# Kernel optimization log

Hardware: AMD Instinct MI355X
Metric: run time of the kernel (lower is better)

Reference implementation:

```python
import jax, jax.numpy as jnp
import numpy as np

D = 1024
M = 32768
B = 4096
TEMP = 1.0
LN_EPS = 1e-5


def setup_inputs() -> dict:
    key = jax.random.key(0)
    ks = jax.random.split(key, 8)
    s = 1.0 / np.sqrt(D)
    return {
        "query": jax.random.normal(ks[0], (B, D), dtype=jnp.float32),
        "mem": jax.random.normal(ks[1], (M, D), dtype=jnp.float32),
        "Wq": jax.random.normal(ks[2], (D, D), dtype=jnp.float32) * s,
        "bq": jax.random.normal(ks[3], (D,), dtype=jnp.float32) * 0.01,
        "Wk": jax.random.normal(ks[4], (D, D), dtype=jnp.float32) * s,
        "bk": jax.random.normal(ks[5], (D,), dtype=jnp.float32) * 0.01,
        "Wv": jax.random.normal(ks[6], (D, D), dtype=jnp.float32) * s,
        "bv": jax.random.normal(ks[7], (D,), dtype=jnp.float32) * 0.01,
        "gamma": jnp.ones((D,), dtype=jnp.float32),
        "beta": jnp.zeros((D,), dtype=jnp.float32),
        "k": 8,
    }


def reference(query, mem, Wq, bq, Wk, bk, Wv, bv, gamma, beta, k):
    d = query.shape[-1]
    # Linear projections (torch Linear: x @ W.T + b)
    q = query @ Wq.T + bq            # [B, d]
    K = mem @ Wk.T + bk              # [M, d]
    V = mem @ Wv.T + bv              # [M, d]
    # Scaled similarity matrix
    sims = (q @ K.T) / (jnp.sqrt(jnp.asarray(d, q.dtype)) * TEMP)  # [B, M]
    # Top-k selection, then irregular gather of V rows
    _, topi = jax.lax.top_k(sims, k)  # [B, k]
    ret = V[topi]                     # [B, k, d]
    # LayerNorm over last dim (elementwise affine, eps=1e-5, biased var)
    mu = jnp.mean(ret, axis=-1, keepdims=True)
    var = jnp.var(ret, axis=-1, keepdims=True)
    return (ret - mu) * jax.lax.rsqrt(var + LN_EPS) * gamma + beta
```

## Files before the change

kernel.cpp:

```cpp
#include <hip/hip_runtime.h>
#include <hip/hip_bf16.h>
#include <math.h>

#define D_DIM 1024
#define B_ROWS 4096
#define M_ROWS 32768
#define TOPK 8
#define TOPC 16
#define TOPB 8
#define NCB (M_ROWS / 128)

#define BM 128
#define BN 64
#define BK 32

typedef __attribute__((ext_vector_type(8))) short bf16x8;
typedef __attribute__((ext_vector_type(4))) float f32x4;

__device__ __forceinline__ unsigned short f32_to_bf16(float f) {
  unsigned int u = __float_as_uint(f);
  unsigned int r = (u + 0x7FFFu + ((u >> 16) & 1u)) >> 16;
  return (unsigned short)r;
}
__device__ __forceinline__ float bf16_to_f32(unsigned short h) {
  return __uint_as_float(((unsigned int)h) << 16);
}
__device__ __forceinline__ void async_copy16(void* lds, const void* g) {
  __builtin_amdgcn_global_load_lds(
      (const __attribute__((address_space(1))) unsigned int*)g,
      (__attribute__((address_space(3))) unsigned int*)lds, 16, 0, 0);
}

template <int N>
__device__ __forceinline__ void insN(float v, int idx,
                                     float* __restrict__ tv,
                                     int* __restrict__ ti) {
  if (v < tv[N - 1]) return;
  if (v == tv[N - 1] && idx > ti[N - 1]) return;
  float cv = v;
  int ci = idx;
#pragma unroll
  for (int p = 0; p < N; ++p) {
    if (cv > tv[p] || (cv == tv[p] && ci < ti[p])) {
      const float t0 = tv[p]; tv[p] = cv; cv = t0;
      const int t1 = ti[p]; ti[p] = ci; ci = t1;
    }
  }
}

__global__ __launch_bounds__(256) void gram_f64(
    const float* __restrict__ Wq, const float* __restrict__ Wk,
    double* __restrict__ G)
{
  __shared__ float sA[32][68];
  __shared__ float sB[32][68];
  const int tid = threadIdx.x;
  const int tx = tid & 15, ty = tid >> 4;
  const int f0 = blockIdx.x * 64;
  const int e0 = blockIdx.y * 64;

  double acc[4][4];
#pragma unroll
  for (int i = 0; i < 4; ++i)
#pragma unroll
    for (int j = 0; j < 4; ++j) acc[i][j] = 0.0;

  for (int k0 = 0; k0 < D_DIM; k0 += 32) {
#pragma unroll
    for (int it = 0; it < 2; ++it) {
      const int L = it * 256 + tid;
      const int kk = L >> 4, c4 = (L & 15) * 4;
      *(float4*)&sA[kk][c4] = *(const float4*)(Wq + (size_t)(k0 + kk) * D_DIM + f0 + c4);
      *(float4*)&sB[kk][c4] = *(const float4*)(Wk + (size_t)(k0 + kk) * D_DIM + e0 + c4);
    }
    __syncthreads();
#pragma unroll
    for (int kk = 0; kk < 32; ++kk) {
      const double a[4] = {sA[kk][ty * 4 + 0], sA[kk][ty * 4 + 1],
                           sA[kk][ty * 4 + 2], sA[kk][ty * 4 + 3]};
      const double b[4] = {sB[kk][tx * 4 + 0], sB[kk][tx * 4 + 1],
                           sB[kk][tx * 4 + 2], sB[kk][tx * 4 + 3]};
#pragma unroll
      for (int i = 0; i < 4; ++i)
#pragma unroll
        for (int j = 0; j < 4; ++j)
          acc[i][j] = fma(a[i], b[j], acc[i][j]);
    }
    __syncthreads();
  }
#pragma unroll
  for (int i = 0; i < 4; ++i)
#pragma unroll
    for (int j = 0; j < 4; ++j)
      G[(size_t)(f0 + ty * 4 + i) * D_DIM + e0 + tx * 4 + j] = acc[i][j];
}

__global__ __launch_bounds__(256) void colred_f64(
    const float* __restrict__ W, const float* __restrict__ v,
    double* __restrict__ outv)
{
  const int c = blockIdx.x * 256 + threadIdx.x;
  double acc = 0.0;
  for (int n = 0; n < D_DIM; ++n)
    acc = fma((double)W[(size_t)n * D_DIM + c], (double)v[n], acc);
  outv[c] = acc;
}

__global__ __launch_bounds__(256) void dot1024_f64(
    const float* __restrict__ a, const float* __restrict__ b,
    double* __restrict__ out)
{
  const int tid = threadIdx.x;
  double acc = 0.0;
#pragma unroll
  for (int i = 0; i < 4; ++i) {
    const int idx = tid * 4 + i;
    acc = fma((double)a[idx], (double)b[idx], acc);
  }
#pragma unroll
  for (int off = 32; off > 0; off >>= 1) acc += __shfl_down(acc, off);
  __shared__ double red[4];
  if ((tid & 63) == 0) red[tid >> 6] = acc;
  __syncthreads();
  if (tid == 0) out[0] = red[0] + red[1] + red[2] + red[3];
}

__global__ __launch_bounds__(256) void qbk_w(
    const float* __restrict__ query, const double* __restrict__ w,
    const double* __restrict__ s0, double* __restrict__ qbk)
{
  const int b = blockIdx.x * 4 + (threadIdx.x >> 6);
  const int lane = threadIdx.x & 63;
  const float* qrow = query + (size_t)b * D_DIM + lane * 16;
  const double* wrow = w + lane * 16;
  double acc = 0.0;
#pragma unroll
  for (int i = 0; i < 16; ++i)
    acc = fma((double)qrow[i], wrow[i], acc);
#pragma unroll
  for (int off = 32; off > 0; off >>= 1) acc += __shfl_down(acc, off);
  if (lane == 0) qbk[b] = acc + s0[0];
}

__global__ __launch_bounds__(256) void uproj_G(
    const float* __restrict__ query, const double* __restrict__ G,
    const double* __restrict__ ubias, double* __restrict__ U)
{
  __shared__ double sAdT[32][130];
  __shared__ double sBd[32][68];
  const int tid = threadIdx.x;
  const int tx = tid & 15, ty = tid >> 4;
  const int row0 = blockIdx.x * 128;
  const int col0 = blockIdx.y * 64;

  double acc[2][4][4];
#pragma unroll
  for (int g = 0; g < 2; ++g)
#pragma unroll
    for (int i = 0; i < 4; ++i)
#pragma unroll
      for (int j = 0; j < 4; ++j) acc[g][i][j] = 0.0;

  for (int k0 = 0; k0 < D_DIM; k0 += 32) {
#pragma unroll
    for (int it = 0; it < 4; ++it) {
      const int L = it * 256 + tid;
      const int rowa = L >> 3, c4 = (L & 7) * 4;
      const float4 v =
          *(const float4*)(query + (size_t)(row0 + rowa) * D_DIM + k0 + c4);
      sAdT[c4 + 0][rowa] = (double)v.x;
      sAdT[c4 + 1][rowa] = (double)v.y;
      sAdT[c4 + 2][rowa] = (double)v.z;
      sAdT[c4 + 3][rowa] = (double)v.w;
    }
#pragma unroll
    for (int it = 0; it < 4; ++it) {
      const int L = it * 256 + tid;
      const int kk = L >> 5, c2 = (L & 31) * 2;
      *(double2*)&sBd[kk][c2] =
          *(const double2*)(G + (size_t)(k0 + kk) * D_DIM + col0 + c2);
    }
    __syncthreads();
#pragma unroll
    for (int kk = 0; kk < 32; ++kk) {
      const double2 p0 = *(const double2*)&sAdT[kk][ty * 4];
      const double2 p1 = *(const double2*)&sAdT[kk][ty * 4 + 2];
      const double2 p2 = *(const double2*)&sAdT[kk][64 + ty * 4];
      const double2 p3 = *(const double2*)&sAdT[kk][64 + ty * 4 + 2];
      const double a0[4] = {p0.x, p0.y, p1.x, p1.y};
      const double a1[4] = {p2.x, p2.y, p3.x, p3.y};
      const double bb[4] = {sBd[kk][tx * 4 + 0], sBd[kk][tx * 4 + 1],
                            sBd[kk][tx * 4 + 2], sBd[kk][tx * 4 + 3]};
#pragma unroll
      for (int i = 0; i < 4; ++i)
#pragma unroll
        for (int j = 0; j < 4; ++j) {
          acc[0][i][j] = fma(a0[i], bb[j], acc[0][i][j]);
          acc[1][i][j] = fma(a1[i], bb[j], acc[1][i][j]);
        }
    }
    __syncthreads();
  }
  const double ub[4] = {ubias[col0 + tx * 4 + 0], ubias[col0 + tx * 4 + 1],
                        ubias[col0 + tx * 4 + 2], ubias[col0 + tx * 4 + 3]};
#pragma unroll
  for (int g = 0; g < 2; ++g)
#pragma unroll
    for (int i = 0; i < 4; ++i) {
      const size_t base = (size_t)(row0 + g * 64 + ty * 4 + i) * D_DIM + col0 + tx * 4;
      *(double2*)(U + base)     = (double2){acc[g][i][0] + ub[0], acc[g][i][1] + ub[1]};
      *(double2*)(U + base + 2) = (double2){acc[g][i][2] + ub[2], acc[g][i][3] + ub[3]};
    }
}

#define SBUF3 12288
__global__ __launch_bounds__(512, 4) void sims_topc_gemm(
    const unsigned short* __restrict__ A, const unsigned short* __restrict__ B,
    float* __restrict__ part_v, int* __restrict__ part_i)
{
  __shared__ unsigned short smem[3 * SBUF3];

  const int tid = threadIdx.x;
  const int lane = tid & 63;
  const int wave = tid >> 6;
  const int wr = wave >> 1;
  const int wc = wave & 1;

  const int bid = blockIdx.x;
  const int x = bid & 7;
  const int t9 = bid >> 3;
  const int cbg = t9 >> 7;
  const int r = (t9 >> 3) & 15;
  const int cbl = t9 & 7;
  const int cb = (x * 4 + cbg) * 8 + cbl;
  const int row0 = r * 256;
  const int col0 = cb * 128;

  const int st_r = lane >> 2;
  const int st_swz = ((lane & 3) ^ ((st_r >> 1) & 3)) * 16;

  auto STAGE = [&](int d, int k0) {
    unsigned short* buf = smem + d * SBUF3;
#pragma unroll
    for (int i = 0; i < 3; ++i) {
      const int seg = wave * 3 + i;
      if (seg < 16) {
        const int grow = row0 + seg * 16 + st_r;
        async_copy16((char*)(buf + seg * 512),
                     (const char*)(A + (size_t)grow * D_DIM + k0) + st_swz);
      } else {
        const int s2 = seg - 16;
        const int grow = col0 + s2 * 16 + st_r;
        async_copy16((char*)(buf + 8192 + s2 * 512),
                     (const char*)(B + (size_t)grow * D_DIM + k0) + st_swz);
      }
    }
  };

  f32x4 acc[4][4];
#pragma unroll
  for (int m = 0; m < 4; ++m)
#pragma unroll
    for (int n = 0; n < 4; ++n) acc[m][n] = (f32x4){0.f, 0.f, 0.f, 0.f};

  auto COMPUTE = [&](int d) {
    const unsigned short* sA = smem + d * SBUF3;
    const unsigned short* sB = sA + 8192;
    bf16x8 af[4], bfr[4];
    const int ch = lane >> 4;
#pragma unroll
    for (int m = 0; m < 4; ++m) {
      const int Ra = wr * 64 + m * 16 + (lane & 15);
      af[m] = *(const bf16x8*)((const char*)sA + Ra * 64 + ((ch ^ ((Ra >> 1) & 3)) * 16));
    }
#pragma unroll
    for (int n = 0; n < 4; ++n) {
      const int Rb = wc * 64 + n * 16 + (lane & 15);
      bfr[n] = *(const bf16x8*)((const char*)sB + Rb * 64 + ((ch ^ ((Rb >> 1) & 3)) * 16));
    }
    __builtin_amdgcn_s_setprio(1);
#pragma unroll
    for (int m = 0; m < 4; ++m)
#pragma unroll
      for (int n = 0; n < 4; ++n)
        acc[m][n] = __builtin_amdgcn_mfma_f32_16x16x32_bf16(af[m], bfr[n], acc[m][n], 0, 0, 0);
    __builtin_amdgcn_s_setprio(0);
  };

  STAGE(0, 0);
  STAGE(1, 32);
  asm volatile("s_waitcnt vmcnt(3)" ::: "memory");
  __builtin_amdgcn_sched_barrier(0);
  __builtin_amdgcn_s_barrier();

  for (int tt = 0; tt < 30; tt += 3) {
    STAGE(2, (tt + 2) * 32);
    COMPUTE(0);
    asm volatile("s_waitcnt vmcnt(3)" ::: "memory");
    __builtin_amdgcn_sched_barrier(0);
    __builtin_amdgcn_s_barrier();

    STAGE(0, (tt + 3) * 32);
    COMPUTE(1);
    asm volatile("s_waitcnt vmcnt(3)" ::: "memory");
    __builtin_amdgcn_sched_barrier(0);
    __builtin_amdgcn_s_barrier();

    STAGE(1, (tt + 4) * 32);
    COMPUTE(2);
    asm volatile("s_waitcnt vmcnt(3)" ::: "memory");
    __builtin_amdgcn_sched_barrier(0);
    __builtin_amdgcn_s_barrier();
  }
  COMPUTE(0);
  asm volatile("s_waitcnt vmcnt(0)" ::: "memory");
  __builtin_amdgcn_sched_barrier(0);
  __builtin_amdgcn_s_barrier();
  COMPUTE(1);
  __builtin_amdgcn_sched_barrier(0);
  __builtin_amdgcn_s_barrier();

#pragma unroll
  for (int m = 0; m < 4; ++m)
#pragma unroll
    for (int n = 0; n < 4; ++n)
#pragma unroll
      for (int rg = 0; rg < 4; ++rg) {
        const int row = wr * 64 + m * 16 + (lane >> 4) * 4 + rg;
        const int colL = wc * 64 + n * 16 + (lane & 15);
        smem[row * 132 + colL] = f32_to_bf16(acc[m][n][rg]);
      }
  __syncthreads();

  {
    const int row = tid & 255;
    const int h = tid >> 8;
    float tv[4];
    int ti_[4];
#pragma unroll
    for (int p = 0; p < 4; ++p) { tv[p] = -INFINITY; ti_[p] = 0; }
    const unsigned short* crow = smem + row * 132 + h * 64;
    const int gcol = col0 + h * 64;
    for (int j = 0; j < 64; j += 4) {
      const ushort4 c4 = *(const ushort4*)(crow + j);
      insN<4>(bf16_to_f32(c4.x), gcol + j + 0, tv, ti_);
      insN<4>(bf16_to_f32(c4.y), gcol + j + 1, tv, ti_);
      insN<4>(bf16_to_f32(c4.z), gcol + j + 2, tv, ti_);
      insN<4>(bf16_to_f32(c4.w), gcol + j + 3, tv, ti_);
    }
    const size_t base = ((size_t)(row0 + row) * NCB + cb) * TOPB + h * 4;
    *(float4*)(part_v + base) = (float4){tv[0], tv[1], tv[2], tv[3]};
    *(int4*)(part_i + base)   = (int4){ti_[0], ti_[1], ti_[2], ti_[3]};
  }
}

__global__ __launch_bounds__(256) void merge_cand256(
    const float* __restrict__ part_v, const int* __restrict__ part_i,
    int* __restrict__ cand)
{
  const int r = blockIdx.x;
  const int tid = threadIdx.x;
  const int lane = tid & 63;
  const int wave = tid >> 6;

  float tv[8];
  int ti[8];
  {
    const size_t base = ((size_t)r * NCB + tid) * TOPB;
    const float4 a0 = *(const float4*)(part_v + base);
    const float4 a1 = *(const float4*)(part_v + base + 4);
    const int4 b0 = *(const int4*)(part_i + base);
    const int4 b1 = *(const int4*)(part_i + base + 4);
    tv[0] = a0.x; tv[1] = a0.y; tv[2] = a0.z; tv[3] = a0.w;
    tv[4] = a1.x; tv[5] = a1.y; tv[6] = a1.z; tv[7] = a1.w;
    ti[0] = b0.x; ti[1] = b0.y; ti[2] = b0.z; ti[3] = b0.w;
    ti[4] = b1.x; ti[5] = b1.y; ti[6] = b1.z; ti[7] = b1.w;
  }
  unsigned rem = 0xFFu;

  __shared__ float wv4[4];
  __shared__ int wi4[4];
  __shared__ int winner;

  for (int p = 0; p < TOPC; ++p) {
    float bv = -INFINITY;
    int bi = 0x7FFFFFFF;
#pragma unroll
    for (int e = 0; e < 8; ++e) {
      const bool alive = (rem >> e) & 1u;
      const float v = tv[e];
      const int ix = ti[e];
      if (alive && (v > bv || (v == bv && ix < bi))) { bv = v; bi = ix; }
    }
#pragma unroll
    for (int off = 32; off > 0; off >>= 1) {
      const float ov = __shfl_down(bv, off);
      const int oi = __shfl_down(bi, off);
      if (ov > bv || (ov == bv && oi < bi)) { bv = ov; bi = oi; }
    }
    if (lane == 0) { wv4[wave] = bv; wi4[wave] = bi; }
    __syncthreads();
    if (tid == 0) {
      float gv = wv4[0];
      int gi = wi4[0];
#pragma unroll
      for (int w = 1; w < 4; ++w)
        if (wv4[w] > gv || (wv4[w] == gv && wi4[w] < gi)) { gv = wv4[w]; gi = wi4[w]; }
      winner = gi;
      cand[(size_t)r * TOPC + p] = gi;
    }
    __syncthreads();
    const int wgi = winner;
#pragma unroll
    for (int e = 0; e < 8; ++e)
      if (ti[e] == wgi) rem &= ~(1u << e);
  }
}

__global__ __launch_bounds__(256) void rescore_topk_u(
    const double* __restrict__ U, const double* __restrict__ qbk,
    const float* __restrict__ mem, const int* __restrict__ cand,
    int* __restrict__ topi)
{
  const int b = blockIdx.x;
  const int tid = threadIdx.x;
  const int wave = tid >> 6;
  const int lane = tid & 63;

  __shared__ double sval[TOPC];
  __shared__ int sidx[TOPC];

  const double* urow = U + (size_t)b * D_DIM + lane * 16;
  double uv[16];
#pragma unroll
  for (int i = 0; i < 8; ++i) {
    const double2 d2 = *(const double2*)(urow + i * 2);
    uv[i * 2] = d2.x;
    uv[i * 2 + 1] = d2.y;
  }
  const double qb = qbk[b];

  for (int c = wave; c < TOPC; c += 4) {
    const int ci = cand[(size_t)b * TOPC + c];
    const float* mrow = mem + (size_t)ci * D_DIM + lane * 16;
    double acc = 0.0;
#pragma unroll
    for (int i = 0; i < 4; ++i) {
      const float4 mv = *(const float4*)(mrow + i * 4);
      acc = fma(uv[i * 4 + 0], (double)mv.x, acc);
      acc = fma(uv[i * 4 + 1], (double)mv.y, acc);
      acc = fma(uv[i * 4 + 2], (double)mv.z, acc);
      acc = fma(uv[i * 4 + 3], (double)mv.w, acc);
    }
#pragma unroll
    for (int off = 32; off > 0; off >>= 1) acc += __shfl_down(acc, off);
    if (lane == 0) { sval[c] = acc + qb; sidx[c] = ci; }
  }
  __syncthreads();

  if (tid == 0) {
    bool used[TOPC];
#pragma unroll
    for (int p = 0; p < TOPC; ++p) used[p] = false;
#pragma unroll
    for (int p = 0; p < TOPK; ++p) {
      int best = -1;
      double bv = 0.0;
      int bi = 0;
      for (int c = 0; c < TOPC; ++c) {
        if (used[c]) continue;
        const double v = sval[c];
        const int ix = sidx[c];
        if (best < 0 || v > bv || (v == bv && ix < bi)) { best = c; bv = v; bi = ix; }
      }
      used[best] = true;
      topi[(size_t)b * TOPK + p] = bi;
    }
  }
}

#define N4_MEM   (M_ROWS * D_DIM / 4)
#define N4_QUERY (B_ROWS * D_DIM / 4)
#define N4_W     (D_DIM * D_DIM / 4)
#define N4_TOTAL (N4_MEM + N4_QUERY + 3 * N4_W)

__global__ __launch_bounds__(256) void cast_all_bf16(
    const float* __restrict__ mem, const float* __restrict__ query,
    const float* __restrict__ Wk, const float* __restrict__ Wv,
    const float* __restrict__ Wq,
    unsigned short* __restrict__ membf, unsigned short* __restrict__ querybf,
    unsigned short* __restrict__ wkbf, unsigned short* __restrict__ wvbf,
    unsigned short* __restrict__ wqbf)
{
  int i = blockIdx.x * 256 + threadIdx.x;
  if (i >= N4_TOTAL) return;
  const float* src;
  unsigned short* dst;
  if (i < N4_MEM) { src = mem; dst = membf; }
  else if ((i -= N4_MEM) < N4_QUERY) { src = query; dst = querybf; }
  else if ((i -= N4_QUERY) < N4_W) { src = Wk; dst = wkbf; }
  else if ((i -= N4_W) < N4_W) { src = Wv; dst = wvbf; }
  else { i -= N4_W; src = Wq; dst = wqbf; }
  const float4 v = *(const float4*)(src + (size_t)i * 4);
  ushort4 o;
  o.x = f32_to_bf16(v.x);
  o.y = f32_to_bf16(v.y);
  o.z = f32_to_bf16(v.z);
  o.w = f32_to_bf16(v.w);
  *(ushort4*)(dst + (size_t)i * 4) = o;
}

__global__ __launch_bounds__(256) void kproj_bf16(
    const unsigned short* __restrict__ A,
    const unsigned short* __restrict__ B,
    const float* __restrict__ bias,
    unsigned short* __restrict__ C)
{
  __shared__ unsigned short smem[2 * 2 * 128 * 32];

  const int tid = threadIdx.x;
  const int lane = tid & 63;
  const int wave = tid >> 6;
  const int wr = wave >> 1, wc = wave & 1;
  const int row0 = blockIdx.x * 128;
  const int col0 = blockIdx.y * 128;

  const int st_r = lane >> 2;
  const int st_swz = ((lane & 3) ^ ((st_r >> 1) & 3)) * 16;

  auto STAGE = [&](int d, int k0) {
    unsigned short* dA = smem + d * (2 * 128 * 32);
    unsigned short* dB = dA + 128 * 32;
#pragma unroll
    for (int i = 0; i < 2; ++i) {
      const int seg = wave * 2 + i;
      const int rr = seg * 16 + st_r;
      async_copy16((char*)dA + seg * 1024,
                   (const char*)(A + (size_t)(row0 + rr) * D_DIM + k0) + st_swz);
      async_copy16((char*)dB + seg * 1024,
                   (const char*)(B + (size_t)(col0 + rr) * D_DIM + k0) + st_swz);
    }
  };

  f32x4 acc[4][4];
#pragma unroll
  for (int m = 0; m < 4; ++m)
#pragma unroll
    for (int n = 0; n < 4; ++n) acc[m][n] = (f32x4){0.f, 0.f, 0.f, 0.f};

  STAGE(0, 0);
  __syncthreads();
  int cur = 0;
  const int ch = lane >> 4;
  for (int t = 0; t < 32; ++t) {
    if (t < 31) STAGE(cur ^ 1, (t + 1) * 32);
    const unsigned short* sA = smem + cur * (2 * 128 * 32);
    const unsigned short* sB = sA + 128 * 32;
    bf16x8 af[4], bfr[4];
#pragma unroll
    for (int m = 0; m < 4; ++m) {
      const int Ra = wr * 64 + m * 16 + (lane & 15);
      af[m] = *(const bf16x8*)((const char*)sA + Ra * 64 + ((ch ^ ((Ra >> 1) & 3)) * 16));
    }
#pragma unroll
    for (int n = 0; n < 4; ++n) {
      const int Rb = wc * 64 + n * 16 + (lane & 15);
      bfr[n] = *(const bf16x8*)((const char*)sB + Rb * 64 + ((ch ^ ((Rb >> 1) & 3)) * 16));
    }
#pragma unroll
    for (int m = 0; m < 4; ++m)
#pragma unroll
      for (int n = 0; n < 4; ++n)
        acc[m][n] = __builtin_amdgcn_mfma_f32_16x16x32_bf16(af[m], bfr[n], acc[m][n], 0, 0, 0);
    __syncthreads();
    cur ^= 1;
  }

#pragma unroll
  for (int n = 0; n < 4; ++n) {
    const int col = col0 + wc * 64 + n * 16 + (lane & 15);
    const float bcol = bias[col];
#pragma unroll
    for (int m = 0; m < 4; ++m)
#pragma unroll
      for (int r = 0; r < 4; ++r) {
        const int row = row0 + wr * 64 + m * 16 + (lane >> 4) * 4 + r;
        C[(size_t)row * D_DIM + col] = f32_to_bf16(acc[m][n][r] + bcol);
      }
  }
}

__global__ __launch_bounds__(256) void gather_ln(
    const unsigned short* __restrict__ V, const int* __restrict__ topi,
    const float* __restrict__ gamma, const float* __restrict__ beta,
    float* __restrict__ out)
{
  const int row = blockIdx.x;
  const int tid = threadIdx.x;
  const int idx = topi[row];
  const unsigned short* src = V + (size_t)idx * D_DIM;
  const ushort4 raw = *(const ushort4*)(src + tid * 4);
  const float v0 = bf16_to_f32(raw.x);
  const float v1 = bf16_to_f32(raw.y);
  const float v2 = bf16_to_f32(raw.z);
  const float v3 = bf16_to_f32(raw.w);
  float s = v0 + v1 + v2 + v3;
  float s2 = v0 * v0 + v1 * v1 + v2 * v2 + v3 * v3;
#pragma unroll
  for (int off = 32; off > 0; off >>= 1) {
    s += __shfl_down(s, off);
    s2 += __shfl_down(s2, off);
  }
  __shared__ float red[8];
  __shared__ float stats[2];
  const int wid = tid >> 6;
  if ((tid & 63) == 0) { red[wid] = s; red[4 + wid] = s2; }
  __syncthreads();
  if (tid == 0) {
    const float S = red[0] + red[1] + red[2] + red[3];
    const float S2 = red[4] + red[5] + red[6] + red[7];
    const float mu = S * (1.0f / D_DIM);
    const float var = S2 * (1.0f / D_DIM) - mu * mu;
    stats[0] = mu;
    stats[1] = rsqrtf(var + 1e-5f);
  }
  __syncthreads();
  const float mu = stats[0], rstd = stats[1];
  const float4 g4 = *(const float4*)(gamma + tid * 4);
  const float4 b4 = *(const float4*)(beta + tid * 4);
  float4 o;
  o.x = (v0 - mu) * rstd * g4.x + b4.x;
  o.y = (v1 - mu) * rstd * g4.y + b4.y;
  o.z = (v2 - mu) * rstd * g4.z + b4.z;
  o.w = (v3 - mu) * rstd * g4.w + b4.w;
  *(float4*)(out + (size_t)row * D_DIM + tid * 4) = o;
}

extern "C" void kernel_launch(void* const* d_in, const int* in_sizes, int n_in,
                              void* d_out, int out_size, void* d_ws, size_t ws_size,
                              hipStream_t stream)
{
  const float* query = (const float*)d_in[0];
  const float* mem   = (const float*)d_in[1];
  const float* Wq    = (const float*)d_in[2];
  const float* bq    = (const float*)d_in[3];
  const float* Wk    = (const float*)d_in[4];
  const float* bk    = (const float*)d_in[5];
  const float* Wv    = (const float*)d_in[6];
  const float* bv    = (const float*)d_in[7];
  const float* gamma = (const float*)d_in[8];
  const float* beta  = (const float*)d_in[9];
  float* out = (float*)d_out;

  char* ws = (char*)d_ws;
  double* u64 = (double*)ws;   ws += (size_t)B_ROWS * D_DIM * sizeof(double);
  double* G = (double*)ws;     ws += (size_t)D_DIM * D_DIM * sizeof(double);
  unsigned short* qbf = (unsigned short*)ws;
  ws += (size_t)B_ROWS * D_DIM * sizeof(unsigned short);
  unsigned short* querybf = (unsigned short*)ws;
  ws += (size_t)B_ROWS * D_DIM * sizeof(unsigned short);
  unsigned short* membf = (unsigned short*)ws;
  ws += (size_t)M_ROWS * D_DIM * sizeof(unsigned short);
  char* Aregion = ws;
  ws += (size_t)M_ROWS * D_DIM * sizeof(unsigned short)
      + 2 * (size_t)B_ROWS * NCB * TOPB * sizeof(float);
  double* wvec = (double*)ws;  ws += (size_t)D_DIM * sizeof(double);
  double* ubias = (double*)ws; ws += (size_t)D_DIM * sizeof(double);
  double* s0 = (double*)ws;    ws += 2 * sizeof(double);
  double* qbk = (double*)ws;   ws += (size_t)B_ROWS * sizeof(double);
  int* cand = (int*)ws;        ws += (size_t)B_ROWS * TOPC * sizeof(int);
  int* topi = (int*)ws;

  unsigned short* Kbf = (unsigned short*)Aregion;
  float* part_v = (float*)(Aregion + (size_t)M_ROWS * D_DIM * sizeof(unsigned short));
  int* part_i = (int*)((char*)part_v + (size_t)B_ROWS * NCB * TOPB * sizeof(float));
  unsigned short* wkbf = (unsigned short*)G;
  unsigned short* wvbf = wkbf + (size_t)D_DIM * D_DIM;
  unsigned short* wqbf = wvbf + (size_t)D_DIM * D_DIM;
  unsigned short* Vbf = (unsigned short*)Aregion;

  gram_f64<<<dim3(16, 16), 256, 0, stream>>>(Wq, Wk, G);
  colred_f64<<<dim3(4), 256, 0, stream>>>(Wq, bk, wvec);
  colred_f64<<<dim3(4), 256, 0, stream>>>(Wk, bq, ubias);
  dot1024_f64<<<dim3(1), 256, 0, stream>>>(bq, bk, s0);
  qbk_w<<<dim3(B_ROWS / 4), 256, 0, stream>>>(query, wvec, s0, qbk);
  uproj_G<<<dim3(B_ROWS / 128, D_DIM / 64), 256, 0, stream>>>(query, G, ubias, u64);

  cast_all_bf16<<<dim3((N4_TOTAL + 255) / 256), 256, 0, stream>>>(
      mem, query, Wk, Wv, Wq, membf, querybf, wkbf, wvbf, wqbf);

  kproj_bf16<<<dim3(M_ROWS / 128, D_DIM / 128), 256, 0, stream>>>(membf, wkbf, bk, Kbf);
  kproj_bf16<<<dim3(B_ROWS / 128, D_DIM / 128), 256, 0, stream>>>(querybf, wqbf, bq, qbf);

  sims_topc_gemm<<<dim3((B_ROWS / 256) * NCB), 512, 0, stream>>>(qbf, Kbf, part_v, part_i);
  merge_cand256<<<dim3(B_ROWS), 256, 0, stream>>>(part_v, part_i, cand);
  rescore_topk_u<<<dim3(B_ROWS), 256, 0, stream>>>(u64, qbk, mem, cand, topi);

  kproj_bf16<<<dim3(M_ROWS / 128, D_DIM / 128), 256, 0, stream>>>(membf, wvbf, bv, Vbf);
  gather_ln<<<dim3(B_ROWS * TOPK), 256, 0, stream>>>(Vbf, topi, gamma, beta, out);
}
```

Measured before the change: 1.257 ms.

## Replace projection GEMM with 256x128-tile, 8-wave, triple-buffered pipelined kernel

Swaps the 128x128 double-buffered bf16 projection GEMM for a 512-thread kernel that computes 256x128 tiles. It uses a three-stage LDS ring with explicit vmcnt waits and raw barriers, so global-to-LDS loads run two steps ahead of the MFMA work, and it raises wave priority around the MFMAs. The larger tile is meant to cut B-operand reloads per output and hide memory latency. It relies on the SBUF3 macro defined elsewhere and on hand-tuned waitcnt counts, which may be fragile.

```diff
diff --git a/kernel.cpp b/kernel.cpp
--- a/kernel.cpp
+++ b/kernel.cpp
@@ -9,10 +9,6 @@
 #define TOPC 16
 #define TOPB 8
 #define NCB (M_ROWS / 128)
-
-#define BM 128
-#define BN 64
-#define BK 32
 
 typedef __attribute__((ext_vector_type(8))) short bf16x8;
 typedef __attribute__((ext_vector_type(4))) float f32x4;
@@ -351,6 +347,119 @@
     const size_t base = ((size_t)(row0 + row) * NCB + cb) * TOPB + h * 4;
     *(float4*)(part_v + base) = (float4){tv[0], tv[1], tv[2], tv[3]};
     *(int4*)(part_i + base)   = (int4){ti_[0], ti_[1], ti_[2], ti_[3]};
+  }
+}
+
+__global__ __launch_bounds__(512, 4) void proj256_bf16(
+    const unsigned short* __restrict__ A,
+    const unsigned short* __restrict__ B,
+    const float* __restrict__ bias,
+    unsigned short* __restrict__ C)
+{
+  __shared__ unsigned short smem[3 * SBUF3];
+
+  const int tid = threadIdx.x;
+  const int lane = tid & 63;
+  const int wave = tid >> 6;
+  const int wr = wave >> 1;
+  const int wc = wave & 1;
+
+  const int row0 = blockIdx.x * 256;
+  const int col0 = blockIdx.y * 128;
+
+  const int st_r = lane >> 2;
+  const int st_swz = ((lane & 3) ^ ((st_r >> 1) & 3)) * 16;
+
+  auto STAGE = [&](int d, int k0) {
+    unsigned short* buf = smem + d * SBUF3;
+#pragma unroll
+    for (int i = 0; i < 3; ++i) {
+      const int seg = wave * 3 + i;
+      if (seg < 16) {
+        const int grow = row0 + seg * 16 + st_r;
+        async_copy16((char*)(buf + seg * 512),
+                     (const char*)(A + (size_t)grow * D_DIM + k0) + st_swz);
+      } else {
+        const int s2 = seg - 16;
+        const int grow = col0 + s2 * 16 + st_r;
+        async_copy16((char*)(buf + 8192 + s2 * 512),
+                     (const char*)(B + (size_t)grow * D_DIM + k0) + st_swz);
+      }
+    }
+  };
+
+  f32x4 acc[4][4];
+#pragma unroll
+  for (int m = 0; m < 4; ++m)
+#pragma unroll
+    for (int n = 0; n < 4; ++n) acc[m][n] = (f32x4){0.f, 0.f, 0.f, 0.f};
+
+  auto COMPUTE = [&](int d) {
+    const unsigned short* sA = smem + d * SBUF3;
+    const unsigned short* sB = sA + 8192;
+    bf16x8 af[4], bfr[4];
+    const int ch = lane >> 4;
+#pragma unroll
+    for (int m = 0; m < 4; ++m) {
+      const int Ra = wr * 64 + m * 16 + (lane & 15);
+      af[m] = *(const bf16x8*)((const char*)sA + Ra * 64 + ((ch ^ ((Ra >> 1) & 3)) * 16));
+    }
+#pragma unroll
+    for (int n = 0; n < 4; ++n) {
+      const int Rb = wc * 64 + n * 16 + (lane & 15);
+      bfr[n] = *(const bf16x8*)((const char*)sB + Rb * 64 + ((ch ^ ((Rb >> 1) & 3)) * 16));
+    }
+    __builtin_amdgcn_s_setprio(1);
+#pragma unroll
+    for (int m = 0; m < 4; ++m)
+#pragma unroll
+      for (int n = 0; n < 4; ++n)
+        acc[m][n] = __builtin_amdgcn_mfma_f32_16x16x32_bf16(af[m], bfr[n], acc[m][n], 0, 0, 0);
+    __builtin_amdgcn_s_setprio(0);
+  };
+
+  STAGE(0, 0);
+  STAGE(1, 32);
+  asm volatile("s_waitcnt vmcnt(3)" ::: "memory");
+  __builtin_amdgcn_sched_barrier(0);
+  __builtin_amdgcn_s_barrier();
+
+  for (int tt = 0; tt < 30; tt += 3) {
+    STAGE(2, (tt + 2) * 32);
+    COMPUTE(0);
+    asm volatile("s_waitcnt vmcnt(3)" ::: "memory");
+    __builtin_amdgcn_sched_barrier(0);
+    __builtin_amdgcn_s_barrier();
+
+    STAGE(0, (tt + 3) * 32);
+    COMPUTE(1);
+    asm volatile("s_waitcnt vmcnt(3)" ::: "memory");
+    __builtin_amdgcn_sched_barrier(0);
+    __builtin_amdgcn_s_barrier();
+
+    STAGE(1, (tt + 4) * 32);
+    COMPUTE(2);
+    asm volatile("s_waitcnt vmcnt(3)" ::: "memory");
+    __builtin_amdgcn_sched_barrier(0);
+    __builtin_amdgcn_s_barrier();
+  }
+  COMPUTE(0);
+  asm volatile("s_waitcnt vmcnt(0)" ::: "memory");
+  __builtin_amdgcn_sched_barrier(0);
+  __builtin_amdgcn_s_barrier();
+  COMPUTE(1);
+
+#pragma unroll
+  for (int n = 0; n < 4; ++n) {
+    const int col = col0 + wc * 64 + n * 16 + (lane & 15);
+    const float bcol = bias[col];
+#pragma unroll
+    for (int m = 0; m < 4; ++m)
+#pragma unroll
+      for (int rg = 0; rg < 4; ++rg) {
+        const int row = row0 + wr * 64 + m * 16 + (lane >> 4) * 4 + rg;
+        C[(size_t)row * D_DIM + col] = f32_to_bf16(acc[m][n][rg] + bcol);
+      }
   }
 }
 
@@ -508,86 +617,6 @@
   o.z = f32_to_bf16(v.z);
   o.w = f32_to_bf16(v.w);
   *(ushort4*)(dst + (size_t)i * 4) = o;
-}
-
-__global__ __launch_bounds__(256) void kproj_bf16(
-    const unsigned short* __restrict__ A,
-    const unsigned short* __restrict__ B,
-    const float* __restrict__ bias,
-    unsigned short* __restrict__ C)
-{
-  __shared__ unsigned short smem[2 * 2 * 128 * 32];
-
-  const int tid = threadIdx.x;
-  const int lane = tid & 63;
-  const int wave = tid >> 6;
-  const int wr = wave >> 1, wc = wave & 1;
-  const int row0 = blockIdx.x * 128;
-  const int col0 = blockIdx.y * 128;
-
-  const int st_r = lane >> 2;
-  const int st_swz = ((lane & 3) ^ ((st_r >> 1) & 3)) * 16;
-
-  auto STAGE = [&](int d, int k0) {
-    unsigned short* dA = smem + d * (2 * 128 * 32);
-    unsigned short* dB = dA + 128 * 32;
-#pragma unroll
-    for (int i = 0; i < 2; ++i) {
-      const int seg = wave * 2 + i;
-      const int rr = seg * 16 + st_r;
-      async_copy16((char*)dA + seg * 1024,
-                   (const char*)(A + (size_t)(row0 + rr) * D_DIM + k0) + st_swz);
-      async_copy16((char*)dB + seg * 1024,
-                   (const char*)(B + (size_t)(col0 + rr) * D_DIM + k0) + st_swz);
-    }
-  };
-
-  f32x4 acc[4][4];
-#pragma unroll
-  for (int m = 0; m < 4; ++m)
-#pragma unroll
-    for (int n = 0; n < 4; ++n) acc[m][n] = (f32x4){0.f, 0.f, 0.f, 0.f};
-
-  STAGE(0, 0);
-  __syncthreads();
-  int cur = 0;
-  const int ch = lane >> 4;
-  for (int t = 0; t < 32; ++t) {
-    if (t < 31) STAGE(cur ^ 1, (t + 1) * 32);
-    const unsigned short* sA = smem + cur * (2 * 128 * 32);
-    const unsigned short* sB = sA + 128 * 32;
-    bf16x8 af[4], bfr[4];
-#pragma unroll
-    for (int m = 0; m < 4; ++m) {
-      const int Ra = wr * 64 + m * 16 + (lane & 15);
-      af[m] = *(const bf16x8*)((const char*)sA + Ra * 64 + ((ch ^ ((Ra >> 1) & 3)) * 16));
-    }
-#pragma unroll
-    for (int n = 0; n < 4; ++n) {
-      const int Rb = wc * 64 + n * 16 + (lane & 15);
-      bfr[n] = *(const bf16x8*)((const char*)sB + Rb * 64 + ((ch ^ ((Rb >> 1) & 3)) * 16));
-    }
-#pragma unroll
-    for (int m = 0; m < 4; ++m)
-#pragma unroll
-      for (int n = 0; n < 4; ++n)
-        acc[m][n] = __builtin_amdgcn_mfma_f32_16x16x32_bf16(af[m], bfr[n], acc[m][n], 0, 0, 0);
-    __syncthreads();
-    cur ^= 1;
-  }
-
-#pragma unroll
-  for (int n = 0; n < 4; ++n) {
-    const int col = col0 + wc * 64 + n * 16 + (lane & 15);
-    const float bcol = bias[col];
-#pragma unroll
-    for (int m = 0; m < 4; ++m)
-#pragma unroll
-      for (int r = 0; r < 4; ++r) {
-        const int row = row0 + wr * 64 + m * 16 + (lane >> 4) * 4 + r;
-        C[(size_t)row * D_DIM + col] = f32_to_bf16(acc[m][n][r] + bcol);
-      }
-  }
 }
 
 __global__ __launch_bounds__(256) void gather_ln(
@@ -689,13 +718,13 @@
   cast_all_bf16<<<dim3((N4_TOTAL + 255) / 256), 256, 0, stream>>>(
       mem, query, Wk, Wv, Wq, membf, querybf, wkbf, wvbf, wqbf);
 
-  kproj_bf16<<<dim3(M_ROWS / 128, D_DIM / 128), 256, 0, stream>>>(membf, wkbf, bk, Kbf);
-  kproj_bf16<<<dim3(B_ROWS / 128, D_DIM / 128), 256, 0, stream>>>(querybf, wqbf, bq, qbf);
+  proj256_bf16<<<dim3(M_ROWS / 256, D_DIM / 128), 512, 0, stream>>>(membf, wkbf, bk, Kbf);
+  proj256_bf16<<<dim3(B_ROWS / 256, D_DIM / 128), 512, 0, stream>>>(querybf, wqbf, bq, qbf);
 
   sims_topc_gemm<<<dim3((B_ROWS / 256) * NCB), 512, 0, stream>>>(qbf, Kbf, part_v, part_i);
   merge_cand256<<<dim3(B_ROWS), 256, 0, stream>>>(part_v, part_i, cand);
   rescore_topk_u<<<dim3(B_ROWS), 256, 0, stream>>>(u64, qbk, mem, cand, topi);
 
-  kproj_bf16<<<dim3(M_ROWS / 128, D_DIM / 128), 256, 0, stream>>>(membf, wvbf, bv, Vbf);
+  proj256_bf16<<<dim3(M_ROWS / 256, D_DIM / 128), 512, 0, stream>>>(membf, wvbf, bv, Vbf);
   gather_ln<<<dim3(B_ROWS * TOPK), 256, 0, stream>>>(Vbf, topi, gamma, beta, out);
 }
```

Measured after the change: 1.248 ms. Within noise of the previous version (-0.7%).
